# Kernel optimization log

Measured on AMD Instinct MI355X. Metric: run time of the kernel, lower is better.

## Reference

```python
import jax, jax.numpy as jnp
import numpy as np

N = 6
DT = 0.01
MARGIN = 0.1
LOWER = jnp.array([-6.28, -6.28, -3.14, -6.28, -6.28, -6.28], dtype=jnp.float32)
UPPER = jnp.array([6.28, 6.28, 3.14, 6.28, 6.28, 6.28], dtype=jnp.float32)
EFFORT = jnp.array([150.0, 150.0, 150.0, 28.0, 28.0, 28.0], dtype=jnp.float32)
TRIL_I, TRIL_J = np.tril_indices(N)


def setup_inputs() -> dict:
    key = jax.random.key(0)
    B = 16384
    ks = jax.random.split(key, 16)
    def lin(kw, kb, out_d, in_d):
        s = 1.0 / np.sqrt(in_d)
        return (jax.random.uniform(kw, (out_d, in_d), jnp.float32, -s, s),
                jax.random.uniform(kb, (out_d,), jnp.float32, -s, s))
    W1L, b1L = lin(ks[0], ks[1], 128, 2 * N)
    W2L, b2L = lin(ks[2], ks[3], 128, 128)
    W3L, b3L = lin(ks[4], ks[5], N * (N + 1) // 2, 128)
    W1V, b1V = lin(ks[6], ks[7], 128, 2 * N)
    W2V, b2V = lin(ks[8], ks[9], 128, 128)
    W3V, b3V = lin(ks[10], ks[11], 1, 128)
    obs = jax.random.normal(ks[12], (B, 2 * N), jnp.float32)
    action = jax.random.normal(ks[13], (B, N), jnp.float32)
    return dict(obs=obs, action=action, W1L=W1L, b1L=b1L, W2L=W2L, b2L=b2L,
                W3L=W3L, b3L=b3L, W1V=W1V, b1V=b1V, W2V=W2V, b2V=b2V,
                W3V=W3V, b3V=b3V)


def reference(obs, action, W1L, b1L, W2L, b2L, W3L, b3L,
              W1V, b1V, W2V, b2V, W3V, b3V):
    sp = jax.nn.softplus

    def trig(q):  # [..., N] -> [..., 2N] interleaved cos/sin
        return jnp.stack([jnp.cos(q), jnp.sin(q)], axis=-1).reshape(q.shape[:-1] + (2 * N,))

    def mass_single(q):  # q: [N] -> M: [N, N]
        t = trig(q)
        h = sp(t @ W1L.T + b1L)
        h = sp(h @ W2L.T + b2L)
        y = sp(h @ W3L.T + b3L)
        L = jnp.zeros((N, N), q.dtype).at[TRIL_I, TRIL_J].set(y)
        return L @ L.T

    def pot_single(q):  # q: [N] -> scalar V
        t = trig(q)
        h = sp(t @ W1V.T + b1V)
        h = sp(h @ W2V.T + b2V)
        return (h @ W3V.T + b3V)[0]

    mass = jax.vmap(mass_single)                    # [B,N,N]
    dmass = jax.vmap(jax.jacrev(mass_single))       # [B,N,N,N] (last axis = d/dq)
    grav = jax.vmap(jax.grad(pot_single))           # [B,N]

    def constraints(q):  # barrier forces; clip branch if any sample of a joint violates
        lo = LOWER + MARGIN
        up = UPPER - MARGIN
        viol = jnp.any((q <= lo) | (q >= up), axis=0)  # [N], per-joint global flag
        clip = jnp.where(q <= lo, EFFORT, jnp.where(q >= up, -EFFORT, 0.0))
        barrier = -5.0 * (1.0 / (q - lo) - 1.0 / (up - q))
        return jnp.where(viol[None, :], clip, barrier)

    def accel(q, qdot, tau):
        M = mass(q)
        dM = dmass(q)  # dM[b,i,j,k] = dM_ij/dq_k
        # Christoffel: C[i,j] = sum_k (dM[i,k]/dq_j - 0.5 dM[k,j]/dq_i) qdot_k
        C = (jnp.einsum('bikj,bk->bij', dM, qdot)
             - 0.5 * jnp.einsum('bkji,bk->bij', dM, qdot))
        c = jnp.einsum('bij,bj->bi', C, qdot)
        g = grav(q)
        f = constraints(q)
        rhs = tau - c - g - f
        return jnp.linalg.solve(M, rhs[..., None])[..., 0]

    q = obs[:, :N]
    qdot = obs[:, N:]
    tau = action * EFFORT

    # RK4
    k1_q = qdot
    k1_qd = accel(q, qdot, tau)
    k2_q = qdot + 0.5 * DT * k1_qd
    k2_qd = accel(q + 0.5 * DT * k1_q, k2_q, tau)
    k3_q = qdot + 0.5 * DT * k2_qd
    k3_qd = accel(q + 0.5 * DT * k2_q, k3_q, tau)
    k4_q = qdot + DT * k3_qd
    k4_qd = accel(q + DT * k3_q, k4_q, tau)

    q_new = q + DT / 6.0 * (k1_q + 2 * k2_q + 2 * k3_q + k4_q)
    qdot_new = qdot + DT / 6.0 * (k1_qd + 2 * k2_qd + 2 * k3_qd + k4_qd)
    q_new = jnp.clip(q_new, LOWER, UPPER)
    return jnp.concatenate([q_new, qdot_new], axis=1)
```

## Files before the change

### kernel.cpp

```cpp
#include <hip/hip_runtime.h>
#include <math.h>

#define BATCH 16384
#define B6 (BATCH*6)
#define DT 0.01f

using half8_t = __attribute__((ext_vector_type(8))) _Float16;
using half4_t = __attribute__((ext_vector_type(4))) _Float16;
using half2_t = __attribute__((ext_vector_type(2))) _Float16;
using f32x4   = __attribute__((ext_vector_type(4))) float;

__device__ __constant__ float c_LOWER[6]  = {-6.28f,-6.28f,-3.14f,-6.28f,-6.28f,-6.28f};
__device__ __constant__ float c_UPPER[6]  = { 6.28f, 6.28f, 3.14f, 6.28f, 6.28f, 6.28f};
__device__ __constant__ float c_EFFORT[6] = {150.0f,150.0f,150.0f,28.0f,28.0f,28.0f};
__device__ __constant__ int   c_ROWOFF[6] = {0,1,3,6,10,15};

__device__ __forceinline__ float sp_f(float z){
  return fmaxf(z,0.0f) + __logf(1.0f + __expf(-fabsf(z)));
}
__device__ __forceinline__ float sig_f(float z){
  return __builtin_amdgcn_rcpf(1.0f + __expf(-z));
}
__device__ __forceinline__ void spsig_f(float z, float& sp, float& sg){
  float e = __expf(-fabsf(z));
  float t = 1.0f + e;
  float r = __builtin_amdgcn_rcpf(t);
  sp = fmaxf(z,0.0f) + __logf(t);
  sg = (z >= 0.0f) ? r : e*r;
}

__device__ __forceinline__ float4 f4all(float v){ return make_float4(v,v,v,v); }
__device__ __forceinline__ void fma4(float4& acc, float w, float4 a){
  acc.x=fmaf(w,a.x,acc.x); acc.y=fmaf(w,a.y,acc.y); acc.z=fmaf(w,a.z,acc.z); acc.w=fmaf(w,a.w,acc.w);
}

__device__ __forceinline__ const float4* chunkc(const float (*arr)[16], int n, int cc){
  return reinterpret_cast<const float4*>(&arr[n][4*(cc ^ ((n>>1)&3))]);
}
__device__ __forceinline__ float& el(float (*arr)[16], int n, int s){
  return arr[n][4*((s>>2) ^ ((n>>1)&3)) + (s&3)];
}

__device__ __forceinline__ f32x4 mfma2(half8_t ah, half8_t al, half8_t bh, f32x4 acc){
  acc = __builtin_amdgcn_mfma_f32_16x16x32_f16(ah, bh, acc, 0,0,0);
  acc = __builtin_amdgcn_mfma_f32_16x16x32_f16(al, bh, acc, 0,0,0);
  return acc;
}
__device__ __forceinline__ f32x4 mfma1(half8_t ah, half8_t bh, f32x4 acc){
  return __builtin_amdgcn_mfma_f32_16x16x32_f16(ah, bh, acc, 0,0,0);
}
__device__ __forceinline__ half8_t ldB(const _Float16 (*B)[136], int n, int q, int quad){
  return *reinterpret_cast<const half8_t*>(&B[n][q*32 + quad*8]);
}
__device__ __forceinline__ void stH2(_Float16 (*Bh)[136], int n, int k2, float a, float b){
  half2_t hi; hi[0]=(_Float16)a; hi[1]=(_Float16)b;
  *reinterpret_cast<half2_t*>(&Bh[n][k2]) = hi;
}
__device__ __forceinline__ void stH4(_Float16 (*Bh)[136], int n, int base, float4 v){
  half4_t hi;
  #pragma unroll
  for (int j=0;j<4;j++) hi[j] = (_Float16)(&v.x)[j];
  *reinterpret_cast<half4_t*>(&Bh[n][base]) = hi;
}

__global__ void __launch_bounds__(256) k_initpre(
    const float* __restrict__ W1L, const float* __restrict__ W2L,
    const float* __restrict__ W3L, const float* __restrict__ W1V,
    const float* __restrict__ W2V, const float* __restrict__ b3L,
    const float* __restrict__ obs,
    float* __restrict__ W1LT, float* __restrict__ W1VT, float* __restrict__ b3Lp,
    _Float16* __restrict__ fragHi, _Float16* __restrict__ fragLo,
    float* __restrict__ q_cur, float* __restrict__ qd_cur, int* __restrict__ viol)
{
  int t = blockIdx.x*256 + threadIdx.x;
  if (t >= 1 && t < 4) viol[t] = 0;
  if (t < 1536){ int i = t/128, k = t%128; W1LT[t] = W1L[k*12+i]; W1VT[t] = W1V[k*12+i]; }
  if (t < 32) b3Lp[t] = (t < 21) ? b3L[t] : 0.0f;
  if (t < 7936){
    int kind, f;
    if (t < 2048){ kind=0; f=t; }
    else if (t < 4096){ kind=1; f=t-2048; }
    else if (t < 6144){ kind=2; f=t-4096; }
    else if (t < 6656){ kind=3; f=t-6144; }
    else if (t < 6912){ kind=4; f=t-6656; }
    else if (t < 7424){ kind=5; f=t-6912; }
    else { kind=6; f=t-7424; }
    int tile, l, m, kq, off;
    if (kind < 5){
      tile = f>>8; int q = (f>>6)&3; l = f&63; m = l&15; kq = 32*q + 8*(l>>4);
      off = (kind==0?0:kind==1?16384:kind==2?32768:kind==3?49152:53248) + f*8;
    } else {
      tile = f>>6; l = f&63; m = l&15; kq = 8*(l>>4);
      off = (kind==5?57344:61440) + f*8;
    }
    #pragma unroll
    for (int e=0;e<8;e++){
      float v;
      int kk = kq + e;
      if (kind==0)      v = W2L[(16*tile+m)*128 + kk];
      else if (kind==1) v = W2V[(16*tile+m)*128 + kk];
      else if (kind==2) v = W2V[kk*128 + (16*tile+m)];
      else if (kind==3){ int r = 16*tile+m; v = (r<21) ? W3L[r*128 + kk] : 0.0f; }
      else if (kind==4) v = (m<12) ? W1V[kk*12 + m] : 0.0f;
      else if (kind==5) v = (kk<12) ? W1L[(16*tile+m)*12 + kk] : 0.0f;
      else              v = (kk<12) ? W1V[(16*tile+m)*12 + kk] : 0.0f;
      _Float16 hi = (_Float16)v;
      _Float16 lo = (_Float16)(v - (float)hi);
      fragHi[off+e] = hi; fragLo[off+e] = lo;
    }
  }
  if (t < BATCH){
    const float* o = obs + t*12;
    unsigned mask = 0;
    #pragma unroll
    for (int i=0;i<6;i++){
      float q = o[i];
      q_cur[t*6+i]=q; qd_cur[t*6+i]=o[6+i];
      float lo = c_LOWER[i]+0.1f, up = c_UPPER[i]-0.1f;
      if (q <= lo || q >= up) mask |= (1u<<i);
    }
    unsigned wm = 0;
    #pragma unroll
    for (int i=0;i<6;i++) if (__ballot((int)((mask>>i)&1u))) wm |= (1u<<i);
    if ((threadIdx.x & 63)==0 && wm) atomicOr(viol, (int)wm);
  }
}

__global__ void __launch_bounds__(256) k_accel(
    int stage, int fold_final,
    const float* __restrict__ obs,
    float* __restrict__ q_cur, float* __restrict__ qd_cur,
    const float* __restrict__ action,
    const float* __restrict__ W1LT, const float* __restrict__ b1L,
    const float* __restrict__ b2L,  const float* __restrict__ b3Lp,
    const float* __restrict__ W1VT, const float* __restrict__ b1V,
    const float* __restrict__ b2V,  const float* __restrict__ W3V,
    const float* __restrict__ W1V,
    const _Float16* __restrict__ fragHi, const _Float16* __restrict__ fragLo,
    int* __restrict__ viol,
    float* __restrict__ kqd_all,
    float* __restrict__ out)
{
  __shared__ alignas(16) _Float16 Bd[2][2][16][136];
  #define Bact Bd[0]
  __shared__ alignas(16) _Float16 tB[16][40];
  __shared__ alignas(16) float sh_t[12][16];
  __shared__ float sh_y[21][17], sh_s3[21][17], sh_dy[42][17], sh_dv[12][17];
  __shared__ float sh_wg[2][6][16];
  __shared__ float sh_qd[6][16], sh_tau[6][16], sh_f[6][16];
  __shared__ float sh_c[6][16], sh_v[6][16];

  float (*sh_s1L)[17] = reinterpret_cast<float(*)[17]>(&Bd[1][0][0][0]);

  const int tid = threadIdx.x;
  const int l = tid & 63;
  const int w = tid >> 6;
  const int lane_n = l & 15;
  const int quad = l >> 4;
  const int base0 = w*16 + quad*4;
  const int base1 = (w+4)*16 + quad*4;
  const int s0 = blockIdx.x * 16;
  const int vm = viol[stage];
  (void)W1V; (void)W1VT;

  const half8_t* fW2Lh  = (const half8_t*)(fragHi);
  const half8_t* fW2Ll  = (const half8_t*)(fragLo);
  const half8_t* fW2Vh  = (const half8_t*)(fragHi + 16384);
  const half8_t* fW2VTh = (const half8_t*)(fragHi + 32768);
  const half8_t* fW3h   = (const half8_t*)(fragHi + 49152);
  const half8_t* fW3l   = (const half8_t*)(fragLo + 49152);
  const half8_t* fW1Th  = (const half8_t*)(fragHi + 53248);
  const half8_t* fW1LAh = (const half8_t*)(fragHi + 57344);
  const half8_t* fW1LAl = (const half8_t*)(fragLo + 57344);
  const half8_t* fW1VAh = (const half8_t*)(fragHi + 61440);

  if (tid < 96){
    int s = tid & 15, i = tid >> 4;
    float q  = q_cur [(s0+s)*6 + i];
    float qd = qd_cur[(s0+s)*6 + i];
    sh_qd[i][s]=qd;
    sh_tau[i][s] = action[(s0+s)*6+i] * c_EFFORT[i];
    float cq = __cosf(q), sq = __sinf(q);
    el(sh_t, 2*i,   s) = cq;
    el(sh_t, 2*i+1, s) = sq;
    tB[s][2*i]   = (_Float16)cq;
    tB[s][2*i+1] = (_Float16)sq;
    float lo = c_LOWER[i]+0.1f, up = c_UPPER[i]-0.1f;
    float barrier = -5.0f*(1.0f/(q-lo) - 1.0f/(up-q));
    float clip = (q<=lo)? c_EFFORT[i] : ((q>=up)? -c_EFFORT[i] : 0.0f);
    sh_f[i][s] = ((vm>>i)&1) ? clip : barrier;
    sh_c[i][s] = 0.0f;
  } else {
    int t2 = tid - 96;
    #pragma unroll
    for (int r=0;r<2;r++){
      int idx = 2*t2 + r;
      if (idx < 320){ int s = idx/20, c = 12 + idx%20; tB[s][c] = (_Float16)0.0f; }
    }
  }
  __syncthreads();

  const half8_t tBfrag = *reinterpret_cast<const half8_t*>(&tB[lane_n][quad*8]);

  {
    f32x4 acc0 = {0.f,0.f,0.f,0.f}, acc1 = {0.f,0.f,0.f,0.f};
    acc0 = mfma2(fW1LAh[w*64+l],     fW1LAl[w*64+l],     tBfrag, acc0);
    acc1 = mfma2(fW1LAh[(w+4)*64+l], fW1LAl[(w+4)*64+l], tBfrag, acc1);
    float4 ba = *reinterpret_cast<const float4*>(b1L + base0);
    float4 bb = *reinterpret_cast<const float4*>(b1L + base1);
    float4 h0, h1;
    #pragma unroll
    for (int j=0;j<4;j++){
      float g;
      spsig_f(acc0[j] + (&ba.x)[j], (&h0.x)[j], g);
      sh_s1L[base0+j][lane_n] = g;
      spsig_f(acc1[j] + (&bb.x)[j], (&h1.x)[j], g);
      sh_s1L[base1+j][lane_n] = g;
    }
    stH4(Bact[0], lane_n, base0, h0);
    stH4(Bact[0], lane_n, base1, h1);
  }
  __syncthreads();

  float4 s1a, s1b;
  #pragma unroll
  for (int j=0;j<4;j++){
    (&s1a.x)[j] = sh_s1L[2*l  ][4*w+j];
    (&s1b.x)[j] = sh_s1L[2*l+1][4*w+j];
  }

  float4 s2a, s2b;
  {
    f32x4 acc0 = {0.f,0.f,0.f,0.f}, acc1 = {0.f,0.f,0.f,0.f};
    #pragma unroll
    for (int q=0;q<4;q++){
      half8_t bh = ldB(Bact[0], lane_n, q, quad);
      acc0 = mfma2(fW2Lh[(w*4+q)*64+l],     fW2Ll[(w*4+q)*64+l],     bh, acc0);
      acc1 = mfma2(fW2Lh[((w+4)*4+q)*64+l], fW2Ll[((w+4)*4+q)*64+l], bh, acc1);
    }
    __syncthreads();
    float4 ba = *reinterpret_cast<const float4*>(b2L + base0);
    float4 bb = *reinterpret_cast<const float4*>(b2L + base1);
    float4 h2a, h2b;
    #pragma unroll
    for (int j=0;j<4;j++){
      spsig_f(acc0[j] + (&ba.x)[j], (&h2a.x)[j], (&s2a.x)[j]);
      spsig_f(acc1[j] + (&bb.x)[j], (&h2b.x)[j], (&s2b.x)[j]);
    }
    stH4(Bact[0], lane_n, base0, h2a);
    stH4(Bact[0], lane_n, base1, h2b);
  }
  __syncthreads();

  if (w < 2){
    f32x4 acc = {0.f,0.f,0.f,0.f};
    #pragma unroll
    for (int q=0;q<4;q++){
      half8_t bh = ldB(Bact[0], lane_n, q, quad);
      acc = mfma2(fW3h[(w*4+q)*64+l], fW3l[(w*4+q)*64+l], bh, acc);
    }
    int rb = w*16 + quad*4;
    #pragma unroll
    for (int j=0;j<4;j++){
      int r = rb + j;
      if (r < 21){
        float z = acc[j] + b3Lp[r];
        float sp, sg;
        spsig_f(z, sp, sg);
        sh_y[r][lane_n]  = sp;
        sh_s3[r][lane_n] = sg;
      }
    }
  }
  __syncthreads();

  if (tid < 96){
    int s = tid & 15, jj = tid >> 4;
    float acc = 0.f;
    for (int i=jj;i<6;i++) acc = fmaf(sh_y[c_ROWOFF[i]+jj][s], sh_qd[i][s], acc);
    sh_v[jj][s] = acc;
  }

  for (int G=0; G<3; ++G){
    #pragma unroll
    for (int d=0; d<2; ++d){
      int g = 2*G + d;
      float2 w0 = *reinterpret_cast<const float2*>(W1LT + (2*g)*128 + 2*l);
      float2 w1 = *reinterpret_cast<const float2*>(W1LT + (2*g+1)*128 + 2*l);
      float4 tc = *chunkc(sh_t, 2*g,   w);
      float4 ts = *chunkc(sh_t, 2*g+1, w);
      #pragma unroll
      for (int j=0;j<4;j++){
        float tcj = (&tc.x)[j], tsj = (&ts.x)[j];
        float d0 = (&s1a.x)[j]*(tcj*w1.x - tsj*w0.x);
        float d1 = (&s1b.x)[j]*(tcj*w1.y - tsj*w0.y);
        stH2(Bd[d][0], 4*w+j, 2*l, d0, d1);
      }
    }
    __syncthreads();
    f32x4 ta00={0.f,0.f,0.f,0.f}, ta01=ta00, ta10=ta00, ta11=ta00;
    #pragma unroll
    for (int q=0;q<4;q++){
      half8_t b0h = ldB(Bd[0][0], lane_n, q, quad);
      half8_t b1h = ldB(Bd[1][0], lane_n, q, quad);
      half8_t a0h = fW2Lh[(w*4+q)*64+l];
      half8_t a1h = fW2Lh[((w+4)*4+q)*64+l];
      ta00 = mfma1(a0h, b0h, ta00);
      ta01 = mfma1(a0h, b1h, ta01);
      ta10 = mfma1(a1h, b0h, ta10);
      ta11 = mfma1(a1h, b1h, ta11);
    }
    __syncthreads();
    {
      float4 v;
      #pragma unroll
      for (int j=0;j<4;j++) (&v.x)[j] = (&s2a.x)[j]*ta00[j];
      stH4(Bd[0][0], lane_n, base0, v);
      #pragma unroll
      for (int j=0;j<4;j++) (&v.x)[j] = (&s2b.x)[j]*ta10[j];
      stH4(Bd[0][0], lane_n, base1, v);
      #pragma unroll
      for (int j=0;j<4;j++) (&v.x)[j] = (&s2a.x)[j]*ta01[j];
      stH4(Bd[1][0], lane_n, base0, v);
      #pragma unroll
      for (int j=0;j<4;j++) (&v.x)[j] = (&s2b.x)[j]*ta11[j];
      stH4(Bd[1][0], lane_n, base1, v);
    }
    __syncthreads();
    {
      int d = w & 1, tt = w >> 1;
      f32x4 acc = {0.f,0.f,0.f,0.f};
      #pragma unroll
      for (int q=0;q<4;q++){
        half8_t bh = ldB(Bd[d][0], lane_n, q, quad);
        acc = mfma1(fW3h[(tt*4+q)*64+l], bh, acc);
      }
      int rb = tt*16 + quad*4;
      #pragma unroll
      for (int j=0;j<4;j++){
        int r = rb + j;
        if (r < 21) sh_dy[d*21 + r][lane_n] = sh_s3[r][lane_n] * acc[j];
      }
    }
    __syncthreads();
    if (tid < 32){
      int s = tid & 15, gg = tid >> 4;
      float qd[6];
      #pragma unroll
      for (int i=0;i<6;i++) qd[i] = sh_qd[i][s];
      float u[6];
      #pragma unroll
      for (int jj=0;jj<6;jj++){
        float acc = 0.f;
        for (int i=jj;i<6;i++) acc = fmaf(sh_dy[gg*21 + c_ROWOFF[i]+jj][s], qd[i], acc);
        u[jj] = acc;
      }
      #pragma unroll
      for (int i=0;i<6;i++){
        float acc = 0.f;
        for (int j=0;j<=i;j++){
          acc = fmaf(sh_dy[gg*21 + c_ROWOFF[i]+j][s], sh_v[j][s], acc);
          acc = fmaf(sh_y [c_ROWOFF[i]+j][s], u[j], acc);
        }
        sh_wg[gg][i][s] = acc;
      }
    }
    __syncthreads();
    if (tid < 96){
      int s = tid & 15, i = tid >> 4;
      float acc = sh_c[i][s];
      acc = fmaf(sh_qd[2*G][s],   sh_wg[0][i][s], acc);
      acc = fmaf(sh_qd[2*G+1][s], sh_wg[1][i][s], acc);
      int gi = i - 2*G;
      if (gi == 0 || gi == 1){
        float r = 0.f;
        #pragma unroll
        for (int j=0;j<6;j++) r = fmaf(sh_qd[j][s], sh_wg[gi][j][s], r);
        acc -= 0.5f*r;
      }
      sh_c[i][s] = acc;
    }
  }

  float4 s1Va, s1Vb;
  {
    f32x4 acc0 = {0.f,0.f,0.f,0.f}, acc1 = {0.f,0.f,0.f,0.f};
    acc0 = mfma1(fW1VAh[w*64+l],     tBfrag, acc0);
    acc1 = mfma1(fW1VAh[(w+4)*64+l], tBfrag, acc1);
    float4 ba = *reinterpret_cast<const float4*>(b1V + base0);
    float4 bb = *reinterpret_cast<const float4*>(b1V + base1);
    float4 h0, h1;
    #pragma unroll
    for (int j=0;j<4;j++){
      spsig_f(acc0[j] + (&ba.x)[j], (&h0.x)[j], (&s1Va.x)[j]);
      spsig_f(acc1[j] + (&bb.x)[j], (&h1.x)[j], (&s1Vb.x)[j]);
    }
    stH4(Bact[0], lane_n, base0, h0);
    stH4(Bact[0], lane_n, base1, h1);
  }
  __syncthreads();
  {
    f32x4 acc0 = {0.f,0.f,0.f,0.f}, acc1 = {0.f,0.f,0.f,0.f};
    #pragma unroll
    for (int q=0;q<4;q++){
      half8_t bh = ldB(Bact[0], lane_n, q, quad);
      acc0 = mfma1(fW2Vh[(w*4+q)*64+l],     bh, acc0);
      acc1 = mfma1(fW2Vh[((w+4)*4+q)*64+l], bh, acc1);
    }
    __syncthreads();
    float4 ba  = *reinterpret_cast<const float4*>(b2V + base0);
    float4 bb  = *reinterpret_cast<const float4*>(b2V + base1);
    float4 w3a = *reinterpret_cast<const float4*>(W3V + base0);
    float4 w3b = *reinterpret_cast<const float4*>(W3V + base1);
    float4 g2a, g2b;
    #pragma unroll
    for (int j=0;j<4;j++){
      (&g2a.x)[j] = sig_f(acc0[j] + (&ba.x)[j]) * (&w3a.x)[j];
      (&g2b.x)[j] = sig_f(acc1[j] + (&bb.x)[j]) * (&w3b.x)[j];
    }
    stH4(Bact[0], lane_n, base0, g2a);
    stH4(Bact[0], lane_n, base1, g2b);
  }
  __syncthreads();
  {
    f32x4 acc0 = {0.f,0.f,0.f,0.f}, acc1 = {0.f,0.f,0.f,0.f};
    #pragma unroll
    for (int q=0;q<4;q++){
      half8_t bh = ldB(Bact[0], lane_n, q, quad);
      acc0 = mfma1(fW2VTh[(w*4+q)*64+l],     bh, acc0);
      acc1 = mfma1(fW2VTh[((w+4)*4+q)*64+l], bh, acc1);
    }
    float4 g1a, g1b;
    #pragma unroll
    for (int j=0;j<4;j++){
      (&g1a.x)[j] = (&s1Va.x)[j] * acc0[j];
      (&g1b.x)[j] = (&s1Vb.x)[j] * acc1[j];
    }
    __syncthreads();
    stH4(Bact[0], lane_n, base0, g1a);
    stH4(Bact[0], lane_n, base1, g1b);
  }
  __syncthreads();
  if (w == 0){
    f32x4 acc = {0.f,0.f,0.f,0.f};
    #pragma unroll
    for (int q=0;q<4;q++){
      half8_t bh = ldB(Bact[0], lane_n, q, quad);
      acc = mfma1(fW1Th[q*64+l], bh, acc);
    }
    int rb = quad*4;
    #pragma unroll
    for (int j=0;j<4;j++){
      int r = rb + j;
      if (r < 12) sh_dv[r][lane_n] = acc[j];
    }
  }
  __syncthreads();
  if (l < 4){
    int s = w*4 + l;
    float Lm[21];
    #pragma unroll
    for (int o=0;o<21;o++) Lm[o] = sh_y[o][s];
    float rhs[6];
    #pragma unroll
    for (int i=0;i<6;i++){
      float grav = fmaf(el(sh_t,2*i,s), sh_dv[2*i+1][s],
                        -(el(sh_t,2*i+1,s)*sh_dv[2*i][s]));
      rhs[i] = sh_tau[i][s] - sh_c[i][s] - grav - sh_f[i][s];
    }
    float z[6];
    #pragma unroll
    for (int i=0;i<6;i++){
      float acc = rhs[i];
      for (int j=0;j<i;j++) acc = fmaf(-Lm[c_ROWOFF[i]+j], z[j], acc);
      z[i] = acc * __builtin_amdgcn_rcpf(Lm[c_ROWOFF[i]+i]);
    }
    float a[6];
    #pragma unroll
    for (int i=5;i>=0;i--){
      float acc = z[i];
      for (int j=i+1;j<6;j++) acc = fmaf(-Lm[c_ROWOFF[j]+i], a[j], acc);
      a[i] = acc * __builtin_amdgcn_rcpf(Lm[c_ROWOFF[i]+i]);
    }
    int b = s0 + s;
    float* kqd_out = kqd_all + stage*B6;
    #pragma unroll
    for (int i=0;i<6;i++) kqd_out[b*6+i] = a[i];

    if (stage < 3){
      const float* o = obs + b*12;
      unsigned mask = 0;
      #pragma unroll
      for (int i=0;i<6;i++){
        float q0=o[i], qd0=o[6+i];
        float q, qd;
        if (stage == 0){
          q  = q0 + 0.5f*DT*qd0;
          qd = qd0 + 0.5f*DT*a[i];
        } else if (stage == 1){
          float k1 = kqd_all[b*6+i];
          q  = q0 + 0.5f*DT*qd0 + 0.25f*DT*DT*k1;
          qd = qd0 + 0.5f*DT*a[i];
        } else {
          float k2 = kqd_all[B6 + b*6+i];
          q  = q0 + DT*qd0 + 0.5f*DT*DT*k2;
          qd = qd0 + DT*a[i];
        }
        q_cur[b*6+i]=q; qd_cur[b*6+i]=qd;
        float lo = c_LOWER[i]+0.1f, up = c_UPPER[i]-0.1f;
        if (q <= lo || q >= up) mask |= (1u<<i);
      }
      if (mask) atomicOr(viol + stage + 1, (int)mask);
    }

    if (fold_final){
      const float* o = obs + b*12;
      float* po = out + b*12;
      #pragma unroll
      for (int i=0;i<6;i++){
        float q0=o[i], qd0=o[6+i];
        float k1=kqd_all[b*6+i], k2=kqd_all[B6+b*6+i], k3=kqd_all[2*B6+b*6+i];
        float qn = q0 + DT*qd0 + (DT*DT/6.0f)*(k1+k2+k3);
        qn = fminf(fmaxf(qn, c_LOWER[i]), c_UPPER[i]);
        po[i] = qn;
        po[6+i] = qd0 + (DT/6.0f)*(k1 + 2.0f*k2 + 2.0f*k3 + a[i]);
      }
    }
  }
  #undef Bact
}

extern "C" void kernel_launch(void* const* d_in, const int* in_sizes, int n_in,
                              void* d_out, int out_size, void* d_ws, size_t ws_size,
                              hipStream_t stream) {
  const float* obs    = (const float*)d_in[0];
  const float* action = (const float*)d_in[1];
  const float* W1L = (const float*)d_in[2];  const float* b1L = (const float*)d_in[3];
  const float* W2L = (const float*)d_in[4];  const float* b2L = (const float*)d_in[5];
  const float* W3L = (const float*)d_in[6];  const float* b3L = (const float*)d_in[7];
  const float* W1V = (const float*)d_in[8];  const float* b1V = (const float*)d_in[9];
  const float* W2V = (const float*)d_in[10]; const float* b2V = (const float*)d_in[11];
  const float* W3V = (const float*)d_in[12];

  float* ws = (float*)d_ws;
  _Float16* fragHi = (_Float16*)ws;
  _Float16* fragLo = fragHi + 65536;
  float* W1LT  = ws + 65536;
  float* W1VT  = W1LT + 1536;
  float* b3Lp  = W1VT + 1536;
  float* q_cur  = b3Lp + 32;
  float* qd_cur = q_cur + B6;
  float* kqd    = qd_cur + B6;
  int*   viol   = (int*)(kqd + 4*B6);

  float* out = (float*)d_out;

  hipMemsetAsync(viol, 0, sizeof(int), stream);
  k_initpre<<<64,256,0,stream>>>(W1L, W2L, W3L, W1V, W2V, b3L, obs,
                                 W1LT, W1VT, b3Lp, fragHi, fragLo,
                                 q_cur, qd_cur, viol);
  for (int s=0; s<4; ++s){
    k_accel<<<1024,256,0,stream>>>(s, (s==3)?1:0, obs, q_cur, qd_cur, action,
        W1LT, b1L, b2L, b3Lp, W1VT, b1V, b2V, W3V, W1V,
        fragHi, fragLo, viol, kqd, out);
  }
}
```

Baseline: 178.1 us.

## Process three derivative directions per group and ping-pong LDS buffers to drop barriers

The Jacobian loop now handles three q-directions per iteration instead of two, so it runs two groups instead of three. That means fewer barrier rounds and more MFMA work issued per B-fragment load. Activation staging now alternates between separate LDS buffers, which removes the intermediate __syncthreads between the MFMA reads and the writes in the forward and potential-gradient passes. Scratch arrays (s1L, dy, wg) are packed into a shared union to fit the extra buffer. This adds register pressure from six accumulators and leaves an uneven wave workload in the W3 pass.

Result: no change. 181.5 us (+1.9%).

```diff
diff --git a/kernel.cpp b/kernel.cpp
--- a/kernel.cpp
+++ b/kernel.cpp
@@ -30,9 +30,6 @@
 }
 
 __device__ __forceinline__ float4 f4all(float v){ return make_float4(v,v,v,v); }
-__device__ __forceinline__ void fma4(float4& acc, float w, float4 a){
-  acc.x=fmaf(w,a.x,acc.x); acc.y=fmaf(w,a.y,acc.y); acc.z=fmaf(w,a.z,acc.z); acc.w=fmaf(w,a.w,acc.w);
-}
 
 __device__ __forceinline__ const float4* chunkc(const float (*arr)[16], int n, int cc){
   return reinterpret_cast<const float4*>(&arr[n][4*(cc ^ ((n>>1)&3))]);
@@ -142,15 +139,16 @@
     float* __restrict__ out)
 {
   __shared__ alignas(16) _Float16 Bd[2][2][16][136];
-  #define Bact Bd[0]
   __shared__ alignas(16) _Float16 tB[16][40];
   __shared__ alignas(16) float sh_t[12][16];
-  __shared__ float sh_y[21][17], sh_s3[21][17], sh_dy[42][17], sh_dv[12][17];
-  __shared__ float sh_wg[2][6][16];
+  __shared__ float sh_y[21][17], sh_s3[21][17], sh_dv[12][17];
+  __shared__ alignas(16) char uS[8704];
   __shared__ float sh_qd[6][16], sh_tau[6][16], sh_f[6][16];
   __shared__ float sh_c[6][16], sh_v[6][16];
 
-  float (*sh_s1L)[17] = reinterpret_cast<float(*)[17]>(&Bd[1][0][0][0]);
+  float (*sh_s1L)[17]   = reinterpret_cast<float(*)[17]>(uS);
+  float (*sh_dy)[17]    = reinterpret_cast<float(*)[17]>(uS);
+  float (*sh_wg)[6][16] = reinterpret_cast<float(*)[6][16]>(uS + 4352);
 
   const int tid = threadIdx.x;
   const int l = tid & 63;
@@ -168,7 +166,6 @@
   const half8_t* fW2Vh  = (const half8_t*)(fragHi + 16384);
   const half8_t* fW2VTh = (const half8_t*)(fragHi + 32768);
   const half8_t* fW3h   = (const half8_t*)(fragHi + 49152);
-  const half8_t* fW3l   = (const half8_t*)(fragLo + 49152);
   const half8_t* fW1Th  = (const half8_t*)(fragHi + 53248);
   const half8_t* fW1LAh = (const half8_t*)(fragHi + 57344);
   const half8_t* fW1LAl = (const half8_t*)(fragLo + 57344);
@@ -217,8 +214,8 @@
       spsig_f(acc1[j] + (&bb.x)[j], (&h1.x)[j], g);
       sh_s1L[base1+j][lane_n] = g;
     }
-    stH4(Bact[0], lane_n, base0, h0);
-    stH4(Bact[0], lane_n, base1, h1);
+    stH4(Bd[0][0], lane_n, base0, h0);
+    stH4(Bd[0][0], lane_n, base1, h1);
   }
   __syncthreads();
 
@@ -234,11 +231,10 @@
     f32x4 acc0 = {0.f,0.f,0.f,0.f}, acc1 = {0.f,0.f,0.f,0.f};
     #pragma unroll
     for (int q=0;q<4;q++){
-      half8_t bh = ldB(Bact[0], lane_n, q, quad);
+      half8_t bh = ldB(Bd[0][0], lane_n, q, quad);
       acc0 = mfma2(fW2Lh[(w*4+q)*64+l],     fW2Ll[(w*4+q)*64+l],     bh, acc0);
       acc1 = mfma2(fW2Lh[((w+4)*4+q)*64+l], fW2Ll[((w+4)*4+q)*64+l], bh, acc1);
     }
-    __syncthreads();
     float4 ba = *reinterpret_cast<const float4*>(b2L + base0);
     float4 bb = *reinterpret_cast<const float4*>(b2L + base1);
     float4 h2a, h2b;
@@ -247,8 +243,8 @@
       spsig_f(acc0[j] + (&ba.x)[j], (&h2a.x)[j], (&s2a.x)[j]);
       spsig_f(acc1[j] + (&bb.x)[j], (&h2b.x)[j], (&s2b.x)[j]);
     }
-    stH4(Bact[0], lane_n, base0, h2a);
-    stH4(Bact[0], lane_n, base1, h2b);
+    stH4(Bd[1][0], lane_n, base0, h2a);
+    stH4(Bd[1][0], lane_n, base1, h2b);
   }
   __syncthreads();
 
@@ -256,8 +252,8 @@
     f32x4 acc = {0.f,0.f,0.f,0.f};
     #pragma unroll
     for (int q=0;q<4;q++){
-      half8_t bh = ldB(Bact[0], lane_n, q, quad);
-      acc = mfma2(fW3h[(w*4+q)*64+l], fW3l[(w*4+q)*64+l], bh, acc);
+      half8_t bh = ldB(Bd[1][0], lane_n, q, quad);
+      acc = mfma2(fW3h[(w*4+q)*64+l], ((const half8_t*)(fragLo + 49152))[(w*4+q)*64+l], bh, acc);
     }
     int rb = w*16 + quad*4;
     #pragma unroll
@@ -281,10 +277,11 @@
     sh_v[jj][s] = acc;
   }
 
-  for (int G=0; G<3; ++G){
-    #pragma unroll
-    for (int d=0; d<2; ++d){
-      int g = 2*G + d;
+  for (int G2=0; G2<2; ++G2){
+    #pragma unroll
+    for (int d=0; d<3; ++d){
+      int g = 3*G2 + d;
+      _Float16 (*Dd)[136] = (d==0)? Bd[0][0] : (d==1)? Bd[0][1] : Bd[1][0];
       float2 w0 = *reinterpret_cast<const float2*>(W1LT + (2*g)*128 + 2*l);
       float2 w1 = *reinterpret_cast<const float2*>(W1LT + (2*g+1)*128 + 2*l);
       float4 tc = *chunkc(sh_t, 2*g,   w);
@@ -294,56 +291,64 @@
         float tcj = (&tc.x)[j], tsj = (&ts.x)[j];
         float d0 = (&s1a.x)[j]*(tcj*w1.x - tsj*w0.x);
         float d1 = (&s1b.x)[j]*(tcj*w1.y - tsj*w0.y);
-        stH2(Bd[d][0], 4*w+j, 2*l, d0, d1);
+        stH2(Dd, 4*w+j, 2*l, d0, d1);
       }
     }
     __syncthreads();
-    f32x4 ta00={0.f,0.f,0.f,0.f}, ta01=ta00, ta10=ta00, ta11=ta00;
+    f32x4 ta[2][3];
+    #pragma unroll
+    for (int r=0;r<2;r++)
+      #pragma unroll
+      for (int d=0;d<3;d++) ta[r][d] = (f32x4){0.f,0.f,0.f,0.f};
     #pragma unroll
     for (int q=0;q<4;q++){
-      half8_t b0h = ldB(Bd[0][0], lane_n, q, quad);
-      half8_t b1h = ldB(Bd[1][0], lane_n, q, quad);
-      half8_t a0h = fW2Lh[(w*4+q)*64+l];
-      half8_t a1h = fW2Lh[((w+4)*4+q)*64+l];
-      ta00 = mfma1(a0h, b0h, ta00);
-      ta01 = mfma1(a0h, b1h, ta01);
-      ta10 = mfma1(a1h, b0h, ta10);
-      ta11 = mfma1(a1h, b1h, ta11);
+      half8_t b0 = ldB(Bd[0][0], lane_n, q, quad);
+      half8_t b1 = ldB(Bd[0][1], lane_n, q, quad);
+      half8_t b2 = ldB(Bd[1][0], lane_n, q, quad);
+      half8_t a0 = fW2Lh[(w*4+q)*64+l];
+      half8_t a1 = fW2Lh[((w+4)*4+q)*64+l];
+      ta[0][0] = mfma1(a0, b0, ta[0][0]);
+      ta[0][1] = mfma1(a0, b1, ta[0][1]);
+      ta[0][2] = mfma1(a0, b2, ta[0][2]);
+      ta[1][0] = mfma1(a1, b0, ta[1][0]);
+      ta[1][1] = mfma1(a1, b1, ta[1][1]);
+      ta[1][2] = mfma1(a1, b2, ta[1][2]);
     }
     __syncthreads();
-    {
+    #pragma unroll
+    for (int d=0;d<3;d++){
+      _Float16 (*Dd)[136] = (d==0)? Bd[0][0] : (d==1)? Bd[0][1] : Bd[1][0];
       float4 v;
       #pragma unroll
-      for (int j=0;j<4;j++) (&v.x)[j] = (&s2a.x)[j]*ta00[j];
-      stH4(Bd[0][0], lane_n, base0, v);
-      #pragma unroll
-      for (int j=0;j<4;j++) (&v.x)[j] = (&s2b.x)[j]*ta10[j];
-      stH4(Bd[0][0], lane_n, base1, v);
-      #pragma unroll
-      for (int j=0;j<4;j++) (&v.x)[j] = (&s2a.x)[j]*ta01[j];
-      stH4(Bd[1][0], lane_n, base0, v);
-      #pragma unroll
-      for (int j=0;j<4;j++) (&v.x)[j] = (&s2b.x)[j]*ta11[j];
-      stH4(Bd[1][0], lane_n, base1, v);
+      for (int j=0;j<4;j++) (&v.x)[j] = (&s2a.x)[j]*ta[0][d][j];
+      stH4(Dd, lane_n, base0, v);
+      #pragma unroll
+      for (int j=0;j<4;j++) (&v.x)[j] = (&s2b.x)[j]*ta[1][d][j];
+      stH4(Dd, lane_n, base1, v);
     }
     __syncthreads();
-    {
-      int d = w & 1, tt = w >> 1;
-      f32x4 acc = {0.f,0.f,0.f,0.f};
-      #pragma unroll
-      for (int q=0;q<4;q++){
-        half8_t bh = ldB(Bd[d][0], lane_n, q, quad);
-        acc = mfma1(fW3h[(tt*4+q)*64+l], bh, acc);
-      }
-      int rb = tt*16 + quad*4;
-      #pragma unroll
-      for (int j=0;j<4;j++){
-        int r = rb + j;
-        if (r < 21) sh_dy[d*21 + r][lane_n] = sh_s3[r][lane_n] * acc[j];
+    #pragma unroll
+    for (int pass=0; pass<2; ++pass){
+      int m = (pass==0) ? w : ((w<2) ? (w+4) : -1);
+      if (m >= 0){
+        int d = m>>1, tt = m&1;
+        const _Float16 (*Dd)[136] = (d==0)? Bd[0][0] : (d==1)? Bd[0][1] : Bd[1][0];
+        f32x4 acc = {0.f,0.f,0.f,0.f};
+        #pragma unroll
+        for (int q=0;q<4;q++){
+          half8_t bh = ldB(Dd, lane_n, q, quad);
+          acc = mfma1(fW3h[(tt*4+q)*64+l], bh, acc);
+        }
+        int rb = tt*16 + quad*4;
+        #pragma unroll
+        for (int j=0;j<4;j++){
+          int r = rb + j;
+          if (r < 21) sh_dy[d*21 + r][lane_n] = sh_s3[r][lane_n] * acc[j];
+        }
       }
     }
     __syncthreads();
-    if (tid < 32){
+    if (tid < 48){
       int s = tid & 15, gg = tid >> 4;
       float qd[6];
       #pragma unroll
@@ -369,10 +374,11 @@
     if (tid < 96){
       int s = tid & 15, i = tid >> 4;
       float acc = sh_c[i][s];
-      acc = fmaf(sh_qd[2*G][s],   sh_wg[0][i][s], acc);
-      acc = fmaf(sh_qd[2*G+1][s], sh_wg[1][i][s], acc);
-      int gi = i - 2*G;
-      if (gi == 0 || gi == 1){
+      #pragma unroll
+      for (int d=0;d<3;d++)
+        acc = fmaf(sh_qd[3*G2+d][s], sh_wg[d][i][s], acc);
+      int gi = i - 3*G2;
+      if (gi >= 0 && gi < 3){
         float r = 0.f;
         #pragma unroll
         for (int j=0;j<6;j++) r = fmaf(sh_qd[j][s], sh_wg[gi][j][s], r);
@@ -395,19 +401,18 @@
       spsig_f(acc0[j] + (&ba.x)[j], (&h0.x)[j], (&s1Va.x)[j]);
       spsig_f(acc1[j] + (&bb.x)[j], (&h1.x)[j], (&s1Vb.x)[j]);
     }
-    stH4(Bact[0], lane_n, base0, h0);
-    stH4(Bact[0], lane_n, base1, h1);
+    stH4(Bd[0][0], lane_n, base0, h0);
+    stH4(Bd[0][0], lane_n, base1, h1);
   }
   __syncthreads();
   {
     f32x4 acc0 = {0.f,0.f,0.f,0.f}, acc1 = {0.f,0.f,0.f,0.f};
     #pragma unroll
     for (int q=0;q<4;q++){
-      half8_t bh = ldB(Bact[0], lane_n, q, quad);
+      half8_t bh = ldB(Bd[0][0], lane_n, q, quad);
       acc0 = mfma1(fW2Vh[(w*4+q)*64+l],     bh, acc0);
       acc1 = mfma1(fW2Vh[((w+4)*4+q)*64+l], bh, acc1);
     }
-    __syncthreads();
     float4 ba  = *reinterpret_cast<const float4*>(b2V + base0);
     float4 bb  = *reinterpret_cast<const float4*>(b2V + base1);
     float4 w3a = *reinterpret_cast<const float4*>(W3V + base0);
@@ -418,15 +423,15 @@
       (&g2a.x)[j] = sig_f(acc0[j] + (&ba.x)[j]) * (&w3a.x)[j];
       (&g2b.x)[j] = sig_f(acc1[j] + (&bb.x)[j]) * (&w3b.x)[j];
     }
-    stH4(Bact[0], lane_n, base0, g2a);
-    stH4(Bact[0], lane_n, base1, g2b);
+    stH4(Bd[1][0], lane_n, base0, g2a);
+    stH4(Bd[1][0], lane_n, base1, g2b);
   }
   __syncthreads();
   {
     f32x4 acc0 = {0.f,0.f,0.f,0.f}, acc1 = {0.f,0.f,0.f,0.f};
     #pragma unroll
     for (int q=0;q<4;q++){
-      half8_t bh = ldB(Bact[0], lane_n, q, quad);
+      half8_t bh = ldB(Bd[1][0], lane_n, q, quad);
       acc0 = mfma1(fW2VTh[(w*4+q)*64+l],     bh, acc0);
       acc1 = mfma1(fW2VTh[((w+4)*4+q)*64+l], bh, acc1);
     }
@@ -436,16 +441,15 @@
       (&g1a.x)[j] = (&s1Va.x)[j] * acc0[j];
       (&g1b.x)[j] = (&s1Vb.x)[j] * acc1[j];
     }
-    __syncthreads();
-    stH4(Bact[0], lane_n, base0, g1a);
-    stH4(Bact[0], lane_n, base1, g1b);
+    stH4(Bd[0][0], lane_n, base0, g1a);
+    stH4(Bd[0][0], lane_n, base1, g1b);
   }
   __syncthreads();
   if (w == 0){
     f32x4 acc = {0.f,0.f,0.f,0.f};
     #pragma unroll
     for (int q=0;q<4;q++){
-      half8_t bh = ldB(Bact[0], lane_n, q, quad);
+      half8_t bh = ldB(Bd[0][0], lane_n, q, quad);
       acc = mfma1(fW1Th[q*64+l], bh, acc);
     }
     int rb = quad*4;
@@ -527,7 +531,6 @@
       }
     }
   }
-  #undef Bact
 }
 
 extern "C" void kernel_launch(void* const* d_in, const int* in_sizes, int n_in,
```
